# Performance work log

Hardware: AMD Instinct MI355X
Metric: run time of the kernel (lower is better)

## Reference

```python
import jax, jax.numpy as jnp
import numpy as np

HEADS = 8
DIM_HEAD = 64

def setup_inputs() -> dict:
    key = jax.random.key(0)
    k1, k2 = jax.random.split(key)
    x = jax.random.normal(k1, (4, 2048, 512), dtype=jnp.float32)
    W_qkv = jax.random.normal(k2, (512, 3 * HEADS * DIM_HEAD), dtype=jnp.float32) * (512 ** -0.5)
    return {"x": x, "W_qkv": W_qkv}

def reference(x, W_qkv):
    b, n, _ = x.shape
    h, d = HEADS, DIM_HEAD
    scale = d ** -0.5
    qkv = x @ W_qkv                                   # [b, n, 3*h*d]
    q, k, v = jnp.split(qkv, 3, axis=-1)
    # 'b n (h d) -> b h n d'
    q = q.reshape(b, n, h, d).transpose(0, 2, 1, 3)
    k = k.reshape(b, n, h, d).transpose(0, 2, 1, 3)
    v = v.reshape(b, n, h, d).transpose(0, 2, 1, 3)
    scores = jnp.einsum('bhid,bhjd->bhij', q, k) * scale
    attn_w = jax.nn.softmax(scores, axis=-1)
    out = jnp.einsum('bhij,bhjd->bhid', attn_w, v)
    # 'b h i d -> b i (h d)'
    return out.transpose(0, 2, 1, 3).reshape(b, n, h * d)
```

## Files before the change

kernel.cpp:

```cpp
#include <hip/hip_runtime.h>

#define BATCH 4
#define NSEQ  2048
#define DMODEL 512
#define NHEAD 8
#define DHEAD 64
#define NQKV  1536

typedef __bf16 bf16x8 __attribute__((ext_vector_type(8)));
typedef __bf16 bf16x4 __attribute__((ext_vector_type(4)));
typedef float  f32x4  __attribute__((ext_vector_type(4)));
typedef short  s16x4  __attribute__((ext_vector_type(4)));

__device__ inline void async16(const __bf16* g, __bf16* l) {
    __builtin_amdgcn_global_load_lds(
        (const __attribute__((address_space(1))) void*)g,
        (__attribute__((address_space(3))) void*)l, 16, 0, 0);
}

__device__ inline f32x4 mfma_pv(s16x4 a, s16x4 b, f32x4 c) {
#if !defined(__HIP_DEVICE_COMPILE__)
    (void)a; (void)b;
    return c;
#elif __has_builtin(__builtin_amdgcn_mfma_f32_16x16x16bf16_1k)
    return __builtin_amdgcn_mfma_f32_16x16x16bf16_1k(a, b, c, 0, 0, 0);
#else
    bf16x4 a4 = __builtin_bit_cast(bf16x4, a);
    bf16x4 b4 = __builtin_bit_cast(bf16x4, b);
    bf16x8 a8 = {}, b8 = {};
    for (int i = 0; i < 4; ++i) { a8[i] = a4[i]; b8[i] = b4[i]; }
    return __builtin_amdgcn_mfma_f32_16x16x32_bf16(a8, b8, c, 0, 0, 0);
#endif
}

#define QSCALE 0.18033688011112042f

__global__ __launch_bounds__(256) void prep_kernel(
    const float* __restrict__ x, const float* __restrict__ W,
    __bf16* __restrict__ xb, __bf16* __restrict__ Wt) {
    __shared__ __bf16 t[64][65];
    const int tid = threadIdx.x;
    if (blockIdx.x < 4096) {
        int idx = blockIdx.x * 256 + tid;
        float4 v = ((const float4*)x)[idx];
        bf16x4 o = {(__bf16)v.x, (__bf16)v.y, (__bf16)v.z, (__bf16)v.w};
        ((bf16x4*)xb)[idx] = o;
        return;
    }
    const int bi = blockIdx.x - 4096;
    const int n0 = (bi % 24) * 64, k0 = (bi / 24) * 64;
    const int cr = tid >> 4;
    const int cc = (tid & 15) * 4;
    for (int p = 0; p < 4; ++p) {
        int r = p * 16 + cr;
        float4 v = *(const float4*)&W[(size_t)(k0 + r) * NQKV + n0 + cc];
        t[r][cc + 0] = (__bf16)v.x; t[r][cc + 1] = (__bf16)v.y;
        t[r][cc + 2] = (__bf16)v.z; t[r][cc + 3] = (__bf16)v.w;
    }
    __syncthreads();
    for (int p = 0; p < 4; ++p) {
        int r = p * 16 + cr;
        bf16x4 o = {t[cc + 0][r], t[cc + 1][r], t[cc + 2][r], t[cc + 3][r]};
        *(bf16x4*)&Wt[(size_t)(n0 + r) * DMODEL + k0 + cc] = o;
    }
}

__global__ __launch_bounds__(256) void qkv_gemm_kernel(
    const __bf16* __restrict__ xb, const __bf16* __restrict__ Wt,
    __bf16* __restrict__ Qw, __bf16* __restrict__ Kw, __bf16* __restrict__ Vw) {
    __shared__ __align__(16) char smem[128 * 136 * 2];
    __bf16* Al = (__bf16*)smem;
    __bf16* Bl = Al + 8192;
    __bf16* T  = (__bf16*)smem;

    const int tid  = threadIdx.x;
    const int w    = tid >> 6;
    const int lane = tid & 63;
    const int quad = lane >> 4;
    const int l15  = lane & 15;
    const int wm   = w >> 1, wn = w & 1;
    const int m0 = blockIdx.x * 128;
    const int n0 = blockIdx.y * 128;
    const int segrow = lane >> 3;
    const int sc = (lane & 7) ^ segrow;

    f32x4 acc[4][4];
    for (int i = 0; i < 4; ++i)
        for (int j = 0; j < 4; ++j)
            acc[i][j] = (f32x4){0.f, 0.f, 0.f, 0.f};

    for (int kt = 0; kt < 8; ++kt) {
        const int k0 = kt * 64;
        for (int i = 0; i < 4; ++i) {
            int seg = w * 4 + i;
            int row = seg * 8 + segrow;
            async16(&xb[(size_t)(m0 + row) * DMODEL + k0 + sc * 8], &Al[seg * 512]);
            async16(&Wt[(size_t)(n0 + row) * DMODEL + k0 + sc * 8], &Bl[seg * 512]);
        }
        __syncthreads();
        for (int kc = 0; kc < 2; ++kc) {
            bf16x8 af[4], bfr[4];
            for (int mb = 0; mb < 4; ++mb) {
                int row = wm * 64 + mb * 16 + l15;
                af[mb] = *(const bf16x8*)&Al[row * 64 + (((kc * 4 + quad) ^ (l15 & 7)) * 8)];
            }
            for (int nb = 0; nb < 4; ++nb) {
                int row = wn * 64 + nb * 16 + l15;
                bfr[nb] = *(const bf16x8*)&Bl[row * 64 + (((kc * 4 + quad) ^ (l15 & 7)) * 8)];
            }
            for (int mb = 0; mb < 4; ++mb)
                for (int nb = 0; nb < 4; ++nb)
                    acc[mb][nb] = __builtin_amdgcn_mfma_f32_16x16x32_bf16(
                        af[mb], bfr[nb], acc[mb][nb], 0, 0, 0);
        }
        __syncthreads();
    }

    const int which = n0 >> 9;
    const int bb  = m0 >> 11;
    const int nq0 = m0 & 2047;

    if (which <= 1) {
        for (int mb = 0; mb < 4; ++mb)
            for (int nb = 0; nb < 4; ++nb)
                for (int r = 0; r < 4; ++r) {
                    int ml = wm * 64 + mb * 16 + quad * 4 + r;
                    int nl = wn * 64 + nb * 16 + l15;
                    float a = acc[mb][nb][r];
                    if (which == 0) a *= QSCALE;
                    T[ml * 136 + nl] = (__bf16)a;
                }
        __syncthreads();
        __bf16* dst = which ? Kw : Qw;
        const int h0 = (n0 & 511) >> 6;
        const int region = tid >> 7;
        const int bh = bb * NHEAD + h0 + region;
        __bf16* base = dst + ((size_t)bh * NSEQ + nq0) * DHEAD;
        for (int i = 0; i < 8; ++i) {
            int chunk = (tid & 127) + i * 128;
            int f = chunk * 8;
            int ml = f >> 6, dd = f & 63;
            bf16x8 v = *(const bf16x8*)&T[ml * 136 + region * 64 + dd];
            *(bf16x8*)&base[ml * 64 + dd] = v;
        }
    } else {
        for (int mb = 0; mb < 4; ++mb)
            for (int nb = 0; nb < 4; ++nb) {
                int nl = wn * 64 + nb * 16 + l15;
                int mlb = wm * 64 + mb * 16 + quad * 4;
                bf16x4 v = {(__bf16)acc[mb][nb][0], (__bf16)acc[mb][nb][1],
                            (__bf16)acc[mb][nb][2], (__bf16)acc[mb][nb][3]};
                *(bf16x4*)&T[nl * 136 + mlb] = v;
            }
        __syncthreads();
        const int hv0 = ((n0 - 1024) & 511) >> 6;
        for (int i = 0; i < 8; ++i) {
            int gc = i * 256 + tid;
            int row = gc >> 4, ch = gc & 15;
            bf16x8 v = *(const bf16x8*)&T[row * 136 + ch * 8];
            int bh = bb * NHEAD + hv0 + (row >> 6);
            int dd = row & 63;
            *(bf16x8*)&Vw[((size_t)bh * DHEAD + dd) * NSEQ + nq0 + ch * 8] = v;
        }
    }
}

__global__ __launch_bounds__(512) void attn_kernel(
    const __bf16* __restrict__ Qw, const __bf16* __restrict__ Kw,
    const __bf16* __restrict__ Vw, float* __restrict__ out) {
    __shared__ __align__(16) char smem[128 * 68 * 4];
    float* Of = (float*)smem;

    const int tid  = threadIdx.x;
    const int w    = tid >> 6;
    const int wg   = w & 3;
    const int half = w >> 2;
    const int lane = tid & 63;
    const int quad = lane >> 4;
    const int l15  = lane & 15;
    const int bh = blockIdx.y;
    const int bb = bh >> 3, h = bh & 7;
    const int q0 = blockIdx.x * 128 + wg * 32;
    const int segrow = lane >> 3;
    const int sc = (lane & 7) ^ segrow;

    __bf16* KL = (__bf16*)(smem + half * 16384);
    __bf16* VL = KL + 4096;

    const __bf16* Qh = Qw + (size_t)bh * NSEQ * DHEAD;
    const __bf16* Kh = Kw + (size_t)bh * NSEQ * DHEAD;
    const __bf16* Vh = Vw + (size_t)bh * DHEAD * NSEQ;

    bf16x8 qf[2][2];
    for (int qb = 0; qb < 2; ++qb)
        for (int kc = 0; kc < 2; ++kc)
            qf[qb][kc] = *(const bf16x8*)&Qh[(size_t)(q0 + qb * 16 + l15) * DHEAD + kc * 32 + quad * 8];

    f32x4 O[4][2];
    float l_st[2] = {0.f, 0.f};
    for (int db = 0; db < 4; ++db)
        for (int qb = 0; qb < 2; ++qb)
            O[db][qb] = (f32x4){0.f, 0.f, 0.f, 0.f};

    for (int it = 0; it < 16; ++it) {
        const int k0 = (half * 16 + it) * 64;
        for (int i = 0; i < 2; ++i) {
            int seg = wg * 2 + i;
            int row = seg * 8 + segrow;
            async16(&Kh[(size_t)(k0 + row) * DHEAD + sc * 8], &KL[seg * 512]);
            async16(&Vh[(size_t)row * NSEQ + k0 + sc * 8], &VL[seg * 512]);
            seg += 8 - wg * 2;
        }
        {
            int seg = 4 + wg;
            int row = seg * 8 + segrow;
            async16(&Kh[(size_t)(k0 + row) * DHEAD + sc * 8], &KL[seg * 512]);
            async16(&Vh[(size_t)row * NSEQ + k0 + sc * 8], &VL[seg * 512]);
        }
        __syncthreads();

        f32x4 s[4][2];
        for (int kb = 0; kb < 4; ++kb)
            for (int qb = 0; qb < 2; ++qb)
                s[kb][qb] = (f32x4){0.f, 0.f, 0.f, 0.f};
        for (int kc = 0; kc < 2; ++kc) {
            bf16x8 ak[4];
            for (int kb = 0; kb < 4; ++kb) {
                int row = kb * 16 + l15;
                ak[kb] = *(const bf16x8*)&KL[row * 64 + (((kc * 4 + quad) ^ (l15 & 7)) * 8)];
            }
            for (int kb = 0; kb < 4; ++kb)
                for (int qb = 0; qb < 2; ++qb)
                    s[kb][qb] = __builtin_amdgcn_mfma_f32_16x16x32_bf16(
                        ak[kb], qf[qb][kc], s[kb][qb], 0, 0, 0);
        }

        s16x4 pb[4][2];
        for (int qb = 0; qb < 2; ++qb) {
            float rsum = 0.f;
            for (int kb = 0; kb < 4; ++kb) {
                bf16x4 t;
                for (int r = 0; r < 4; ++r) {
                    float p = __builtin_amdgcn_exp2f(s[kb][qb][r]);
                    rsum += p;
                    t[r] = (__bf16)p;
                }
                pb[kb][qb] = __builtin_bit_cast(s16x4, t);
            }
            rsum += __shfl_xor(rsum, 16);
            rsum += __shfl_xor(rsum, 32);
            l_st[qb] += rsum;
        }

        for (int kb = 0; kb < 4; ++kb) {
            s16x4 av[4];
            for (int db = 0; db < 4; ++db) {
                int d = db * 16 + l15;
                int g = kb * 2 + (quad >> 1);
                av[db] = *(const s16x4*)&VL[(d >> 3) * 512 + (d & 7) * 64 +
                                            ((g ^ (d & 7)) * 8) + (quad & 1) * 4];
            }
            for (int db = 0; db < 4; ++db)
                for (int qb = 0; qb < 2; ++qb)
                    O[db][qb] = mfma_pv(av[db], pb[kb][qb], O[db][qb]);
        }
        __syncthreads();
    }

    if (half == 0) {
        for (int qb = 0; qb < 2; ++qb) {
            int q = wg * 32 + qb * 16 + l15;
            for (int db = 0; db < 4; ++db)
                *(f32x4*)&Of[q * 68 + db * 16 + quad * 4] = O[db][qb];
            if (quad == 0) Of[q * 68 + 64] = l_st[qb];
        }
    }
    __syncthreads();
    if (half == 1) {
        for (int qb = 0; qb < 2; ++qb) {
            int q = wg * 32 + qb * 16 + l15;
            float inv = 1.f / (l_st[qb] + Of[q * 68 + 64]);
            for (int db = 0; db < 4; ++db) {
                f32x4 v = *(const f32x4*)&Of[q * 68 + db * 16 + quad * 4];
                v = (v + O[db][qb]) * inv;
                *(f32x4*)&Of[q * 68 + db * 16 + quad * 4] = v;
            }
        }
    }
    __syncthreads();
    const int nqb = blockIdx.x * 128;
    for (int i = 0; i < 4; ++i) {
        int gc = i * 512 + tid;
        int row = gc >> 4, ch = gc & 15;
        f32x4 v = *(const f32x4*)&Of[row * 68 + ch * 4];
        *(f32x4*)&out[((size_t)(bb * NSEQ + nqb + row)) * DMODEL + h * DHEAD + ch * 4] = v;
    }
}

extern "C" void kernel_launch(void* const* d_in, const int* in_sizes, int n_in,
                              void* d_out, int out_size, void* d_ws, size_t ws_size,
                              hipStream_t stream) {
    const float* x = (const float*)d_in[0];
    const float* W = (const float*)d_in[1];
    float* out = (float*)d_out;

    __bf16* wsp = (__bf16*)d_ws;
    __bf16* xb = wsp;
    __bf16* Wt = xb + 4194304;
    __bf16* Qw = Wt + 786432;
    __bf16* Kw = Qw + 4194304;
    __bf16* Vw = Kw + 4194304;

    prep_kernel<<<4288, 256, 0, stream>>>(x, W, xb, Wt);
    qkv_gemm_kernel<<<dim3(64, 12), 256, 0, stream>>>(xb, Wt, Qw, Kw, Vw);
    attn_kernel<<<dim3(16, 32), 512, 0, stream>>>(Qw, Kw, Vw, out);
}
```

Baseline: 148.6 us.

## Fuse x conversion into QKV GEMM, enlarge GEMM tile, double-buffer attention K/V

The fp32-to-bf16 conversion of x moves out of the prep kernel and into the QKV GEMM, which now loads x directly and converts it in registers before writing to LDS. This removes one full read and write of the bf16 copy of x. The GEMM block grows to 512 threads covering 256 rows, and its epilogue is split into two phases so the output tile still fits in shared memory. The attention kernel now double-buffers K/V tiles so the next load overlaps compute, and it defers the row-sum shuffle reduction to after the loop. The cost is synchronous fp32 loads in the GEMM and larger LDS use in attention, which may lower occupancy.

```diff
diff --git a/kernel.cpp b/kernel.cpp
--- a/kernel.cpp
+++ b/kernel.cpp
@@ -16,6 +16,15 @@
     __builtin_amdgcn_global_load_lds(
         (const __attribute__((address_space(1))) void*)g,
         (__attribute__((address_space(3))) void*)l, 16, 0, 0);
+}
+
+__device__ inline bf16x8 cvt8(const float* __restrict__ p) {
+    float4 a = *(const float4*)p;
+    float4 b = *(const float4*)(p + 4);
+    bf16x8 r;
+    r[0] = (__bf16)a.x; r[1] = (__bf16)a.y; r[2] = (__bf16)a.z; r[3] = (__bf16)a.w;
+    r[4] = (__bf16)b.x; r[5] = (__bf16)b.y; r[6] = (__bf16)b.z; r[7] = (__bf16)b.w;
+    return r;
 }
 
 __device__ inline f32x4 mfma_pv(s16x4 a, s16x4 b, f32x4 c) {
@@ -36,18 +45,10 @@
 #define QSCALE 0.18033688011112042f
 
 __global__ __launch_bounds__(256) void prep_kernel(
-    const float* __restrict__ x, const float* __restrict__ W,
-    __bf16* __restrict__ xb, __bf16* __restrict__ Wt) {
+    const float* __restrict__ W, __bf16* __restrict__ Wt) {
     __shared__ __bf16 t[64][65];
     const int tid = threadIdx.x;
-    if (blockIdx.x < 4096) {
-        int idx = blockIdx.x * 256 + tid;
-        float4 v = ((const float4*)x)[idx];
-        bf16x4 o = {(__bf16)v.x, (__bf16)v.y, (__bf16)v.z, (__bf16)v.w};
-        ((bf16x4*)xb)[idx] = o;
-        return;
-    }
-    const int bi = blockIdx.x - 4096;
+    const int bi = blockIdx.x;
     const int n0 = (bi % 24) * 64, k0 = (bi / 24) * 64;
     const int cr = tid >> 4;
     const int cc = (tid & 15) * 4;
@@ -65,12 +66,12 @@
     }
 }
 
-__global__ __launch_bounds__(256) void qkv_gemm_kernel(
-    const __bf16* __restrict__ xb, const __bf16* __restrict__ Wt,
+__global__ __launch_bounds__(512) void qkv_gemm_kernel(
+    const float* __restrict__ x, const __bf16* __restrict__ Wt,
     __bf16* __restrict__ Qw, __bf16* __restrict__ Kw, __bf16* __restrict__ Vw) {
-    __shared__ __align__(16) char smem[128 * 136 * 2];
+    __shared__ __align__(16) char smem[49152];
     __bf16* Al = (__bf16*)smem;
-    __bf16* Bl = Al + 8192;
+    __bf16* Bl = Al + 16384;
     __bf16* T  = (__bf16*)smem;
 
     const int tid  = threadIdx.x;
@@ -79,7 +80,7 @@
     const int quad = lane >> 4;
     const int l15  = lane & 15;
     const int wm   = w >> 1, wn = w & 1;
-    const int m0 = blockIdx.x * 128;
+    const int m0 = blockIdx.x * 256;
     const int n0 = blockIdx.y * 128;
     const int segrow = lane >> 3;
     const int sc = (lane & 7) ^ segrow;
@@ -91,18 +92,28 @@
 
     for (int kt = 0; kt < 8; ++kt) {
         const int k0 = kt * 64;
-        for (int i = 0; i < 4; ++i) {
-            int seg = w * 4 + i;
+        for (int i = 0; i < 2; ++i) {
+            int seg = w * 2 + i;
             int row = seg * 8 + segrow;
-            async16(&xb[(size_t)(m0 + row) * DMODEL + k0 + sc * 8], &Al[seg * 512]);
             async16(&Wt[(size_t)(n0 + row) * DMODEL + k0 + sc * 8], &Bl[seg * 512]);
         }
+        bf16x8 avs[4];
+        int aoff[4];
+        for (int p = 0; p < 4; ++p) {
+            int g = p * 512 + tid;
+            int row = g >> 3, ch = g & 7;
+            avs[p] = cvt8(&x[(size_t)(m0 + row) * DMODEL + k0 + ch * 8]);
+            aoff[p] = (row >> 3) * 512 + ((row & 7) * 8 + (ch ^ (row & 7))) * 8;
+        }
+        for (int p = 0; p < 4; ++p)
+            *(bf16x8*)&Al[aoff[p]] = avs[p];
         __syncthreads();
         for (int kc = 0; kc < 2; ++kc) {
             bf16x8 af[4], bfr[4];
             for (int mb = 0; mb < 4; ++mb) {
                 int row = wm * 64 + mb * 16 + l15;
-                af[mb] = *(const bf16x8*)&Al[row * 64 + (((kc * 4 + quad) ^ (l15 & 7)) * 8)];
+                af[mb] = *(const bf16x8*)&Al[(row >> 3) * 512 +
+                    ((row & 7) * 8 + ((kc * 4 + quad) ^ (row & 7))) * 8];
             }
             for (int nb = 0; nb < 4; ++nb) {
                 int row = wn * 64 + nb * 16 + l15;
@@ -120,55 +131,60 @@
     const int bb  = m0 >> 11;
     const int nq0 = m0 & 2047;
 
-    if (which <= 1) {
-        for (int mb = 0; mb < 4; ++mb)
-            for (int nb = 0; nb < 4; ++nb)
-                for (int r = 0; r < 4; ++r) {
-                    int ml = wm * 64 + mb * 16 + quad * 4 + r;
-                    int nl = wn * 64 + nb * 16 + l15;
-                    float a = acc[mb][nb][r];
-                    if (which == 0) a *= QSCALE;
-                    T[ml * 136 + nl] = (__bf16)a;
-                }
+    for (int ph = 0; ph < 2; ++ph) {
+        if (which <= 1) {
+            if ((wm >> 1) == ph)
+                for (int mb = 0; mb < 4; ++mb)
+                    for (int nb = 0; nb < 4; ++nb)
+                        for (int r = 0; r < 4; ++r) {
+                            int ml = (wm & 1) * 64 + mb * 16 + quad * 4 + r;
+                            int nl = wn * 64 + nb * 16 + l15;
+                            float a = acc[mb][nb][r];
+                            if (which == 0) a *= QSCALE;
+                            T[ml * 136 + nl] = (__bf16)a;
+                        }
+            __syncthreads();
+            __bf16* dst = which ? Kw : Qw;
+            const int h0 = (n0 & 511) >> 6;
+            const int region = tid >> 8;
+            const int bh = bb * NHEAD + h0 + region;
+            __bf16* base = dst + ((size_t)bh * NSEQ + nq0 + ph * 128) * DHEAD;
+            for (int i = 0; i < 4; ++i) {
+                int chunk = (tid & 255) + i * 256;
+                int f = chunk * 8;
+                int ml = f >> 6, dd = f & 63;
+                bf16x8 v = *(const bf16x8*)&T[ml * 136 + region * 64 + dd];
+                *(bf16x8*)&base[ml * 64 + dd] = v;
+            }
+        } else {
+            if ((wm >> 1) == ph)
+                for (int mb = 0; mb < 4; ++mb)
+                    for (int nb = 0; nb < 4; ++nb) {
+                        int nl = wn * 64 + nb * 16 + l15;
+                        int mlb = (wm & 1) * 64 + mb * 16 + quad * 4;
+                        bf16x4 v = {(__bf16)acc[mb][nb][0], (__bf16)acc[mb][nb][1],
+                                    (__bf16)acc[mb][nb][2], (__bf16)acc[mb][nb][3]};
+                        *(bf16x4*)&T[nl * 136 + mlb] = v;
+                    }
+            __syncthreads();
+            const int hv0 = ((n0 - 1024) & 511) >> 6;
+            for (int i = 0; i < 4; ++i) {
+                int gc = i * 512 + tid;
+                int row = gc >> 4, ch = gc & 15;
+                bf16x8 v = *(const bf16x8*)&T[row * 136 + ch * 8];
+                int bh = bb * NHEAD + hv0 + (row >> 6);
+                int dd = row & 63;
+                *(bf16x8*)&Vw[((size_t)bh * DHEAD + dd) * NSEQ + nq0 + ph * 128 + ch * 8] = v;
+            }
+        }
         __syncthreads();
-        __bf16* dst = which ? Kw : Qw;
-        const int h0 = (n0 & 511) >> 6;
-        const int region = tid >> 7;
-        const int bh = bb * NHEAD + h0 + region;
-        __bf16* base = dst + ((size_t)bh * NSEQ + nq0) * DHEAD;
-        for (int i = 0; i < 8; ++i) {
-            int chunk = (tid & 127) + i * 128;
-            int f = chunk * 8;
-            int ml = f >> 6, dd = f & 63;
-            bf16x8 v = *(const bf16x8*)&T[ml * 136 + region * 64 + dd];
-            *(bf16x8*)&base[ml * 64 + dd] = v;
-        }
-    } else {
-        for (int mb = 0; mb < 4; ++mb)
-            for (int nb = 0; nb < 4; ++nb) {
-                int nl = wn * 64 + nb * 16 + l15;
-                int mlb = wm * 64 + mb * 16 + quad * 4;
-                bf16x4 v = {(__bf16)acc[mb][nb][0], (__bf16)acc[mb][nb][1],
-                            (__bf16)acc[mb][nb][2], (__bf16)acc[mb][nb][3]};
-                *(bf16x4*)&T[nl * 136 + mlb] = v;
-            }
-        __syncthreads();
-        const int hv0 = ((n0 - 1024) & 511) >> 6;
-        for (int i = 0; i < 8; ++i) {
-            int gc = i * 256 + tid;
-            int row = gc >> 4, ch = gc & 15;
-            bf16x8 v = *(const bf16x8*)&T[row * 136 + ch * 8];
-            int bh = bb * NHEAD + hv0 + (row >> 6);
-            int dd = row & 63;
-            *(bf16x8*)&Vw[((size_t)bh * DHEAD + dd) * NSEQ + nq0 + ch * 8] = v;
-        }
     }
 }
 
 __global__ __launch_bounds__(512) void attn_kernel(
     const __bf16* __restrict__ Qw, const __bf16* __restrict__ Kw,
     const __bf16* __restrict__ Vw, float* __restrict__ out) {
-    __shared__ __align__(16) char smem[128 * 68 * 4];
+    __shared__ __align__(16) char smem[65536];
     float* Of = (float*)smem;
 
     const int tid  = threadIdx.x;
@@ -184,8 +200,7 @@
     const int segrow = lane >> 3;
     const int sc = (lane & 7) ^ segrow;
 
-    __bf16* KL = (__bf16*)(smem + half * 16384);
-    __bf16* VL = KL + 4096;
+    __bf16* HB = (__bf16*)smem + half * 16384;
 
     const __bf16* Qh = Qw + (size_t)bh * NSEQ * DHEAD;
     const __bf16* Kh = Kw + (size_t)bh * NSEQ * DHEAD;
@@ -202,22 +217,24 @@
         for (int qb = 0; qb < 2; ++qb)
             O[db][qb] = (f32x4){0.f, 0.f, 0.f, 0.f};
 
-    for (int it = 0; it < 16; ++it) {
+    auto stage = [&](int it, int b) {
         const int k0 = (half * 16 + it) * 64;
+        __bf16* KL = HB + b * 8192;
+        __bf16* VL = KL + 4096;
         for (int i = 0; i < 2; ++i) {
             int seg = wg * 2 + i;
             int row = seg * 8 + segrow;
             async16(&Kh[(size_t)(k0 + row) * DHEAD + sc * 8], &KL[seg * 512]);
             async16(&Vh[(size_t)row * NSEQ + k0 + sc * 8], &VL[seg * 512]);
-            seg += 8 - wg * 2;
-        }
-        {
-            int seg = 4 + wg;
-            int row = seg * 8 + segrow;
-            async16(&Kh[(size_t)(k0 + row) * DHEAD + sc * 8], &KL[seg * 512]);
-            async16(&Vh[(size_t)row * NSEQ + k0 + sc * 8], &VL[seg * 512]);
-        }
+        }
+    };
+
+    stage(0, 0);
+    for (int it = 0; it < 16; ++it) {
         __syncthreads();
+        if (it < 15) stage(it + 1, (it + 1) & 1);
+        const __bf16* Kb = HB + (it & 1) * 8192;
+        const __bf16* Vb = Kb + 4096;
 
         f32x4 s[4][2];
         for (int kb = 0; kb < 4; ++kb)
@@ -227,7 +244,7 @@
             bf16x8 ak[4];
             for (int kb = 0; kb < 4; ++kb) {
                 int row = kb * 16 + l15;
-                ak[kb] = *(const bf16x8*)&KL[row * 64 + (((kc * 4 + quad) ^ (l15 & 7)) * 8)];
+                ak[kb] = *(const bf16x8*)&Kb[row * 64 + (((kc * 4 + quad) ^ (l15 & 7)) * 8)];
             }
             for (int kb = 0; kb < 4; ++kb)
                 for (int qb = 0; qb < 2; ++qb)
@@ -247,8 +264,6 @@
                 }
                 pb[kb][qb] = __builtin_bit_cast(s16x4, t);
             }
-            rsum += __shfl_xor(rsum, 16);
-            rsum += __shfl_xor(rsum, 32);
             l_st[qb] += rsum;
         }
 
@@ -257,16 +272,21 @@
             for (int db = 0; db < 4; ++db) {
                 int d = db * 16 + l15;
                 int g = kb * 2 + (quad >> 1);
-                av[db] = *(const s16x4*)&VL[(d >> 3) * 512 + (d & 7) * 64 +
+                av[db] = *(const s16x4*)&Vb[(d >> 3) * 512 + (d & 7) * 64 +
                                             ((g ^ (d & 7)) * 8) + (quad & 1) * 4];
             }
             for (int db = 0; db < 4; ++db)
                 for (int qb = 0; qb < 2; ++qb)
                     O[db][qb] = mfma_pv(av[db], pb[kb][qb], O[db][qb]);
         }
-        __syncthreads();
-    }
-
+    }
+
+    for (int qb = 0; qb < 2; ++qb) {
+        l_st[qb] += __shfl_xor(l_st[qb], 16);
+        l_st[qb] += __shfl_xor(l_st[qb], 32);
+    }
+
+    __syncthreads();
     if (half == 0) {
         for (int qb = 0; qb < 2; ++qb) {
             int q = wg * 32 + qb * 16 + l15;
@@ -305,13 +325,12 @@
     float* out = (float*)d_out;
 
     __bf16* wsp = (__bf16*)d_ws;
-    __bf16* xb = wsp;
-    __bf16* Wt = xb + 4194304;
+    __bf16* Wt = wsp;
     __bf16* Qw = Wt + 786432;
     __bf16* Kw = Qw + 4194304;
     __bf16* Vw = Kw + 4194304;
 
-    prep_kernel<<<4288, 256, 0, stream>>>(x, W, xb, Wt);
-    qkv_gemm_kernel<<<dim3(64, 12), 256, 0, stream>>>(xb, Wt, Qw, Kw, Vw);
+    prep_kernel<<<192, 256, 0, stream>>>(W, Wt);
+    qkv_gemm_kernel<<<dim3(32, 12), 512, 0, stream>>>(x, Wt, Qw, Kw, Vw);
     attn_kernel<<<dim3(16, 32), 512, 0, stream>>>(Qw, Kw, Vw, out);
 }
```

After: 136.9 us. 1.09x faster.
